# Optimization experiments

Measured on AMD Instinct MI355X. Metric: run time of the kernel, lower is better.

Reference implementation:

```python
import jax, jax.numpy as jnp
import numpy as np

DM = 1024        # model dim
E = 32           # totalexperts = expertsets*nexperts = 8*4
FE = 128         # expertsize
T = 4            # sparsity = nexperts (tokens per group)
EPS_TIEBREAK = 1e-6


def setup_inputs() -> dict:
    key = jax.random.key(0)
    k0, k1, k2, k3 = jax.random.split(key, 4)
    x = jax.random.normal(k0, (4, 4096, DM), dtype=jnp.float32)
    # fan_in-style inits matching misc.get_init_weight / get_init_bias
    controller = jax.random.normal(k1, (DM, E), dtype=jnp.float32) / np.float32(np.sqrt(DM))
    f1 = jax.random.normal(k2, (DM, E, FE), dtype=jnp.float32) / np.float32(np.sqrt(DM))
    bias = jnp.zeros((E, FE), dtype=jnp.float32)
    f2 = jax.random.normal(k3, (E, FE, DM), dtype=jnp.float32) / np.float32(np.sqrt(E * FE / T))
    return {"x": x, "controller": controller, "f1": f1, "bias": bias, "f2": f2}


def reference(x, controller, f1, bias, f2):
    B, S, d = x.shape
    t = T
    g = S // t
    # '... (b t) d -> ... b t d'
    grouped = x.reshape(B, g, t, d)
    # controller logits: '... t d, d e -> ... t e'
    logits = jnp.einsum('bgtd,de->bgte', grouped, controller)
    # deterministic tie-break offset over the t (slot) axis
    logits = logits + jnp.linspace(0.0, EPS_TIEBREAK, t, dtype=logits.dtype)[:, None]
    # softmax over dim=1 (group axis) as in original
    probs = jax.nn.softmax(logits, axis=1)
    # hard argmax mask over dim=-3 (group axis), scaled by soft probs
    perm = (logits == jnp.max(logits, axis=1, keepdims=True)).astype(x.dtype) * probs
    # expert up-projection with soft permutation: '... t d, d e f, ... t e -> ... e f'
    inner = jnp.einsum('bgtd,def,bgte->bgef', grouped, f1, perm)
    inner = jax.nn.relu(inner + bias)
    # expert down-projection: '... e f, e f d -> ... e d'
    inter = jnp.einsum('bgef,efd->bged', inner, f2)
    # unpermute: '... e d, ... t e -> ... t d'
    res = jnp.einsum('bged,bgte->bgtd', inter, perm)
    return res.reshape(B, S, d)
```

## Files before the change

### kernel.cpp

```cpp
#include <hip/hip_runtime.h>
#include <math.h>


#define DM   1024
#define NE   32
#define FE   128
#define T4   4
#define SS   4096
#define NGRP 1024
#define NROW 512
#define LP_STRIDE (NROW * NGRP)
#define VP_OFF   524288

__global__ __launch_bounds__(128, 2)
void k_logits(const float* __restrict__ x, const float* __restrict__ ctrl,
              float* __restrict__ Lp, float* __restrict__ out)
{
    const int m      = blockIdx.x;
    const int ks     = blockIdx.y;
    const int tid    = threadIdx.x;
    const int base_s = m * 128;
    const int b      = base_s >> 12;
    const int g0     = (base_s & 4095) >> 2;

    __shared__ float xT[64 * 132];
    __shared__ float cs[64 * 32];

    const int tq = tid & 31;
    const int eg = tid >> 5;

    float acc[4][8];
#pragma unroll
    for (int i = 0; i < 4; ++i)
#pragma unroll
        for (int j = 0; j < 8; ++j) acc[i][j] = 0.f;

    const int srow = tid >> 4;
    const int scol = tid & 15;

    for (int kit = 0; kit < 4; ++kit) {
        const int k0 = ks * 256 + kit * 64;
        __syncthreads();
#pragma unroll
        for (int p = 0; p < 16; ++p) {
            const int row = p * 8 + srow;
            const float4 v = *(const float4*)(x + (size_t)(base_s + row) * DM + k0 + scol * 4);
            const int d = scol * 4;
            xT[(d + 0) * 132 + row] = v.x;
            xT[(d + 1) * 132 + row] = v.y;
            xT[(d + 2) * 132 + row] = v.z;
            xT[(d + 3) * 132 + row] = v.w;
        }
        {
            const float4* cg = (const float4*)(ctrl + (size_t)k0 * NE);
            float4* cl = (float4*)cs;
            cl[tid]       = cg[tid];
            cl[tid + 128] = cg[tid + 128];
            cl[tid + 256] = cg[tid + 256];
            cl[tid + 384] = cg[tid + 384];
        }
        __syncthreads();

#pragma unroll 4
        for (int d = 0; d < 64; ++d) {
            const float4 xv = *(const float4*)(xT + d * 132 + tq * 4);
            const float4 c0 = *(const float4*)(cs + d * 32 + eg * 8);
            const float4 c1 = *(const float4*)(cs + d * 32 + eg * 8 + 4);
            const float xa[4] = { xv.x, xv.y, xv.z, xv.w };
            const float ca[8] = { c0.x, c0.y, c0.z, c0.w, c1.x, c1.y, c1.z, c1.w };
#pragma unroll
            for (int i = 0; i < 4; ++i)
#pragma unroll
                for (int j = 0; j < 8; ++j) acc[i][j] += xa[i] * ca[j];
        }
    }

    {
        float* Lb = Lp + (size_t)ks * LP_STRIDE;
        const int g = g0 + tq;
#pragma unroll
        for (int i = 0; i < 4; ++i)
#pragma unroll
            for (int j = 0; j < 8; ++j) {
                const int row = (b * T4 + i) * NE + eg * 8 + j;
                Lb[(size_t)row * NGRP + g] = acc[i][j];
            }
    }

    {
        const float4 z = make_float4(0.f, 0.f, 0.f, 0.f);
        float4* o4 = (float4*)(out + (size_t)(base_s + ks * 32) * DM);
#pragma unroll 8
        for (int i = tid; i < 32 * DM / 4; i += 128) o4[i] = z;
    }
}

__global__ __launch_bounds__(64)
void k_route(float* __restrict__ Lp)
{
    const int r    = blockIdx.x;
    const int lane = threadIdx.x;
    const float* L0 = Lp + (size_t)r * NGRP;

    float mx = -INFINITY, s = 0.f;
    int gm = 0;
#pragma unroll
    for (int c = 0; c < 4; ++c) {
        const int g0c = c * 256 + lane * 4;
        const float4 v0 = *(const float4*)(L0 + g0c);
        const float4 v1 = *(const float4*)(L0 + 1 * LP_STRIDE + g0c);
        const float4 v2 = *(const float4*)(L0 + 2 * LP_STRIDE + g0c);
        const float4 v3 = *(const float4*)(L0 + 3 * LP_STRIDE + g0c);
        const float l[4] = { v0.x + v1.x + v2.x + v3.x,
                             v0.y + v1.y + v2.y + v3.y,
                             v0.z + v1.z + v2.z + v3.z,
                             v0.w + v1.w + v2.w + v3.w };
#pragma unroll
        for (int j = 0; j < 4; ++j) {
            const float lv = l[j];
            if (lv > mx) { s = s * __expf(mx - lv) + 1.f; mx = lv; gm = g0c + j; }
            else         { s += __expf(lv - mx); }
        }
    }
#pragma unroll
    for (int off = 1; off < 64; off <<= 1) {
        const float m2 = __shfl_xor(mx, off);
        const float s2 = __shfl_xor(s, off);
        const int   g2 = __shfl_xor(gm, off);
        const float mn = fmaxf(mx, m2);
        s  = s * __expf(mx - mn) + s2 * __expf(m2 - mn);
        gm = (m2 > mx) ? g2 : ((m2 == mx && g2 < gm) ? g2 : gm);
        mx = mn;
    }
    if (lane == 0) {
        ((int*)Lp)[(size_t)r * NGRP] = gm;
        Lp[(size_t)r * NGRP + 1] = 1.f / s;
    }
}

__global__ __launch_bounds__(256, 2)
void k_up(const float* __restrict__ x, const float* __restrict__ f1,
          float* __restrict__ ws)
{
    const int e   = blockIdx.x & 31;
    const int dc  = blockIdx.x >> 5;
    const int tid = threadIdx.x;

    __shared__ float xs[16 * 68];
    __shared__ int   gS[16];

    if (tid < 16) {
        const int r = tid * NE + e;
        gS[tid] = ((const int*)ws)[(size_t)r * NGRP];
    }
    __syncthreads();

    {
        const int row = tid >> 4;
        const int f4c = tid & 15;
        const int bq = row >> 2, t = row & 3;
        const int s = bq * SS + gS[row] * 4 + t;
        const float4 v = *(const float4*)(x + (size_t)s * DM + dc * 64 + f4c * 4);
        xs[row * 68 + f4c * 4 + 0] = v.x;
        xs[row * 68 + f4c * 4 + 1] = v.y;
        xs[row * 68 + f4c * 4 + 2] = v.z;
        xs[row * 68 + f4c * 4 + 3] = v.w;
    }
    __syncthreads();

    const int f4 = tid & 31;
    const int rw = tid >> 5;
    const float* f1p = f1 + (size_t)(dc * 64) * (NE * FE) + e * FE + f4 * 4;
    const float* x0 = xs + rw * 68;
    const float* x1 = xs + (rw + 8) * 68;

    float a0[4] = {0.f, 0.f, 0.f, 0.f}, a1[4] = {0.f, 0.f, 0.f, 0.f};
#pragma unroll 16
    for (int dl = 0; dl < 64; ++dl) {
        const float4 w4 = *(const float4*)(f1p + (size_t)dl * (NE * FE));
        const float xa = x0[dl], xb = x1[dl];
        a0[0] += xa * w4.x; a0[1] += xa * w4.y; a0[2] += xa * w4.z; a0[3] += xa * w4.w;
        a1[0] += xb * w4.x; a1[1] += xb * w4.y; a1[2] += xb * w4.z; a1[3] += xb * w4.w;
    }

    float* Vp = ws + VP_OFF + (size_t)(dc * 32 + e) * (16 * FE);
    *(float4*)(Vp + rw       * FE + f4 * 4) = make_float4(a0[0], a0[1], a0[2], a0[3]);
    *(float4*)(Vp + (rw + 8) * FE + f4 * 4) = make_float4(a1[0], a1[1], a1[2], a1[3]);
}

__global__ __launch_bounds__(256, 2)
void k_down(const float* __restrict__ f2, const float* __restrict__ bias,
            const float* __restrict__ ws, float* __restrict__ out)
{
    const int e   = blockIdx.x & 31;
    const int dt  = (blockIdx.x >> 5) & 7;
    const int rh  = blockIdx.x >> 8;
    const int tid = threadIdx.x;

    __shared__ float vv[8 * 132];
    __shared__ float hs[8 * 132];
    __shared__ int   gS[8];
    __shared__ float pS[8];

    if (tid < 8) {
        const int r = (rh * 8 + tid) * NE + e;
        gS[tid] = ((const int*)ws)[(size_t)r * NGRP];
        pS[tid] = ws[(size_t)r * NGRP + 1];
    }

    {
        const float* Vp = ws + VP_OFF;
        const int row = tid >> 5, f4 = tid & 31;
        float4 s = make_float4(0.f, 0.f, 0.f, 0.f);
#pragma unroll
        for (int dc = 0; dc < 16; ++dc) {
            const float4 v = *(const float4*)(Vp + (size_t)(dc * 32 + e) * (16 * FE)
                                                 + (rh * 8 + row) * FE + f4 * 4);
            s.x += v.x; s.y += v.y; s.z += v.z; s.w += v.w;
        }
        *(float4*)(vv + row * 132 + f4 * 4) = s;
    }
    __syncthreads();

    {
#pragma unroll
        for (int q = 0; q < 4; ++q) {
            const int idx = tid + q * 256;
            const int row = idx >> 7, f = idx & 127;
            const int qb = row & ~3;
            float u = bias[e * FE + f];
#pragma unroll
            for (int t2 = 0; t2 < T4; ++t2)
                if (gS[qb + t2] == gS[row]) u += pS[qb + t2] * vv[(qb + t2) * 132 + f];
            hs[row * 132 + f] = pS[row] * fmaxf(u, 0.f);
        }
    }
    __syncthreads();

    const int d4 = tid & 31;
    const int rw = tid >> 5;
    const float* f2p = f2 + (size_t)e * FE * DM + dt * 128 + d4 * 4;
    const float* hp  = hs + rw * 132;

    float a[4] = {0.f, 0.f, 0.f, 0.f};
#pragma unroll 16
    for (int f = 0; f < FE; ++f) {
        const float4 w4 = *(const float4*)(f2p + (size_t)f * DM);
        const float ha = hp[f];
        a[0] += ha * w4.x; a[1] += ha * w4.y; a[2] += ha * w4.z; a[3] += ha * w4.w;
    }

    const int grow = rh * 8 + rw;
    const int bq = grow >> 2, t = grow & 3;
    float* orow = out + ((size_t)(bq * SS + gS[rw] * 4 + t)) * DM + dt * 128 + d4 * 4;
    atomicAdd(orow + 0, a[0]);
    atomicAdd(orow + 1, a[1]);
    atomicAdd(orow + 2, a[2]);
    atomicAdd(orow + 3, a[3]);
}

extern "C" void kernel_launch(void* const* d_in, const int* in_sizes, int n_in,
                              void* d_out, int out_size, void* d_ws, size_t ws_size,
                              hipStream_t stream)
{
    const float* x    = (const float*)d_in[0];
    const float* ctrl = (const float*)d_in[1];
    const float* f1   = (const float*)d_in[2];
    const float* bias = (const float*)d_in[3];
    const float* f2   = (const float*)d_in[4];
    float* out = (float*)d_out;
    float* ws  = (float*)d_ws;

    k_logits<<<dim3(128, 4), 128, 0, stream>>>(x, ctrl, ws, out);
    k_route <<<dim3(512),     64, 0, stream>>>(ws);
    k_up    <<<dim3(512),    256, 0, stream>>>(x, f1, ws);
    k_down  <<<dim3(512),    256, 0, stream>>>(f2, bias, ws, out);
}
```

Before: 202.3 us.

## Fuse four MoE stages into one cooperative kernel with grid syncs

Replaces the four separate launches (logits, route, up-projection, down-projection) with one cooperative kernel of 512 blocks x 256 threads that separates the stages with grid.sync(). The stage buffers share shared memory through a union. The logits stage is re-tiled for 256 threads with a 4x4 per-thread accumulator. The route stage now uses 4 waves per row with a cross-wave reduction in shared memory. The goal is to remove launch overhead and gaps between kernels, at the cost of grid-wide barrier latency and a cooperative launch that needs all 512 blocks resident at once.

```diff
diff --git a/kernel.cpp b/kernel.cpp
--- a/kernel.cpp
+++ b/kernel.cpp
@@ -1,5 +1,8 @@
 #include <hip/hip_runtime.h>
+#include <hip/hip_cooperative_groups.h>
 #include <math.h>
+
+namespace cg = cooperative_groups;
 
 
 #define DM   1024
@@ -12,101 +15,106 @@
 #define LP_STRIDE (NROW * NGRP)
 #define VP_OFF   524288
 
-__global__ __launch_bounds__(128, 2)
-void k_logits(const float* __restrict__ x, const float* __restrict__ ctrl,
-              float* __restrict__ Lp, float* __restrict__ out)
+struct SM1 { float xT[64 * 132]; float cs[64 * 32]; };
+struct SM2 { float rmx[4]; float rs[4]; int rgm[4]; };
+struct SM3 { float xs[16 * 68]; int gS[16]; };
+struct SM4 { float vv[8 * 132]; float hs[8 * 132]; int gS[8]; float pS[8]; };
+union SMU { SM1 p1; SM2 p2; SM3 p3; SM4 p4; };
+
+__global__ __launch_bounds__(256, 2)
+void k_fused(const float* __restrict__ x, const float* __restrict__ ctrl,
+             const float* __restrict__ f1, const float* __restrict__ bias,
+             const float* __restrict__ f2, float* __restrict__ ws,
+             float* __restrict__ out)
 {
-    const int m      = blockIdx.x;
-    const int ks     = blockIdx.y;
-    const int tid    = threadIdx.x;
-    const int base_s = m * 128;
-    const int b      = base_s >> 12;
-    const int g0     = (base_s & 4095) >> 2;
-
-    __shared__ float xT[64 * 132];
-    __shared__ float cs[64 * 32];
-
-    const int tq = tid & 31;
-    const int eg = tid >> 5;
-
-    float acc[4][8];
-#pragma unroll
-    for (int i = 0; i < 4; ++i)
-#pragma unroll
-        for (int j = 0; j < 8; ++j) acc[i][j] = 0.f;
-
-    const int srow = tid >> 4;
-    const int scol = tid & 15;
-
-    for (int kit = 0; kit < 4; ++kit) {
-        const int k0 = ks * 256 + kit * 64;
-        __syncthreads();
-#pragma unroll
-        for (int p = 0; p < 16; ++p) {
-            const int row = p * 8 + srow;
-            const float4 v = *(const float4*)(x + (size_t)(base_s + row) * DM + k0 + scol * 4);
-            const int d = scol * 4;
-            xT[(d + 0) * 132 + row] = v.x;
-            xT[(d + 1) * 132 + row] = v.y;
-            xT[(d + 2) * 132 + row] = v.z;
-            xT[(d + 3) * 132 + row] = v.w;
-        }
-        {
-            const float4* cg = (const float4*)(ctrl + (size_t)k0 * NE);
-            float4* cl = (float4*)cs;
-            cl[tid]       = cg[tid];
-            cl[tid + 128] = cg[tid + 128];
-            cl[tid + 256] = cg[tid + 256];
-            cl[tid + 384] = cg[tid + 384];
-        }
-        __syncthreads();
-
+    __shared__ SMU sm;
+    cg::grid_group grid = cg::this_grid();
+    const int bid = blockIdx.x;
+    const int tid = threadIdx.x;
+
+    {
+        const int m      = bid >> 2;
+        const int ks     = bid & 3;
+        const int base_s = m * 128;
+        const int b      = base_s >> 12;
+        const int g0     = (base_s & 4095) >> 2;
+
+        const int tq = tid & 31;
+        const int eg = tid >> 5;
+
+        float acc[4][4];
+#pragma unroll
+        for (int i = 0; i < 4; ++i)
+#pragma unroll
+            for (int j = 0; j < 4; ++j) acc[i][j] = 0.f;
+
+        const int row0 = tid >> 2;
+        const int f4i  = tid & 3;
+
+        for (int kit = 0; kit < 4; ++kit) {
+            const int k0 = ks * 256 + kit * 64;
+            __syncthreads();
+#pragma unroll
+            for (int rr = 0; rr < 2; ++rr) {
+                const int row = row0 + rr * 64;
+                const float* xp = x + (size_t)(base_s + row) * DM + k0;
+#pragma unroll
+                for (int cr = 0; cr < 4; ++cr) {
+                    const int col = f4i + cr * 4;
+                    const float4 v = *(const float4*)(xp + col * 4);
+                    const int d = col * 4;
+                    sm.p1.xT[(d + 0) * 132 + row] = v.x;
+                    sm.p1.xT[(d + 1) * 132 + row] = v.y;
+                    sm.p1.xT[(d + 2) * 132 + row] = v.z;
+                    sm.p1.xT[(d + 3) * 132 + row] = v.w;
+                }
+            }
+            {
+                const float4* cg4 = (const float4*)(ctrl + (size_t)k0 * NE);
+                float4* cl = (float4*)sm.p1.cs;
+                cl[tid]       = cg4[tid];
+                cl[tid + 256] = cg4[tid + 256];
+            }
+            __syncthreads();
+#pragma unroll 8
+            for (int d = 0; d < 64; ++d) {
+                const float4 xv = *(const float4*)(sm.p1.xT + d * 132 + tq * 4);
+                const float4 cv = *(const float4*)(sm.p1.cs + d * 32 + eg * 4);
+                const float xa[4] = { xv.x, xv.y, xv.z, xv.w };
+                const float ca[4] = { cv.x, cv.y, cv.z, cv.w };
+#pragma unroll
+                for (int i = 0; i < 4; ++i)
+#pragma unroll
+                    for (int j = 0; j < 4; ++j) acc[i][j] += xa[i] * ca[j];
+            }
+        }
+
+        {
+            float* Lb = ws + (size_t)ks * LP_STRIDE;
+            const int g = g0 + tq;
+#pragma unroll
+            for (int i = 0; i < 4; ++i)
+#pragma unroll
+                for (int j = 0; j < 4; ++j) {
+                    const int row = (b * T4 + i) * NE + eg * 4 + j;
+                    Lb[(size_t)row * NGRP + g] = acc[i][j];
+                }
+        }
+
+        {
+            const float4 z = make_float4(0.f, 0.f, 0.f, 0.f);
+            float4* o4 = (float4*)(out + (size_t)(base_s + ks * 32) * DM);
 #pragma unroll 4
-        for (int d = 0; d < 64; ++d) {
-            const float4 xv = *(const float4*)(xT + d * 132 + tq * 4);
-            const float4 c0 = *(const float4*)(cs + d * 32 + eg * 8);
-            const float4 c1 = *(const float4*)(cs + d * 32 + eg * 8 + 4);
-            const float xa[4] = { xv.x, xv.y, xv.z, xv.w };
-            const float ca[8] = { c0.x, c0.y, c0.z, c0.w, c1.x, c1.y, c1.z, c1.w };
-#pragma unroll
-            for (int i = 0; i < 4; ++i)
-#pragma unroll
-                for (int j = 0; j < 8; ++j) acc[i][j] += xa[i] * ca[j];
-        }
-    }
-
-    {
-        float* Lb = Lp + (size_t)ks * LP_STRIDE;
-        const int g = g0 + tq;
-#pragma unroll
-        for (int i = 0; i < 4; ++i)
-#pragma unroll
-            for (int j = 0; j < 8; ++j) {
-                const int row = (b * T4 + i) * NE + eg * 8 + j;
-                Lb[(size_t)row * NGRP + g] = acc[i][j];
-            }
-    }
-
-    {
-        const float4 z = make_float4(0.f, 0.f, 0.f, 0.f);
-        float4* o4 = (float4*)(out + (size_t)(base_s + ks * 32) * DM);
-#pragma unroll 8
-        for (int i = tid; i < 32 * DM / 4; i += 128) o4[i] = z;
-    }
-}
-
-__global__ __launch_bounds__(64)
-void k_route(float* __restrict__ Lp)
-{
-    const int r    = blockIdx.x;
-    const int lane = threadIdx.x;
-    const float* L0 = Lp + (size_t)r * NGRP;
-
-    float mx = -INFINITY, s = 0.f;
-    int gm = 0;
-#pragma unroll
-    for (int c = 0; c < 4; ++c) {
-        const int g0c = c * 256 + lane * 4;
+            for (int i = tid; i < 32 * DM / 4; i += 256) o4[i] = z;
+        }
+    }
+
+    grid.sync();
+
+    {
+        const int r = bid;
+        const float* L0 = ws + (size_t)r * NGRP;
+        const int g0c = tid * 4;
         const float4 v0 = *(const float4*)(L0 + g0c);
         const float4 v1 = *(const float4*)(L0 + 1 * LP_STRIDE + g0c);
         const float4 v2 = *(const float4*)(L0 + 2 * LP_STRIDE + g0c);
@@ -115,148 +123,154 @@
                              v0.y + v1.y + v2.y + v3.y,
                              v0.z + v1.z + v2.z + v3.z,
                              v0.w + v1.w + v2.w + v3.w };
+        float mx = -INFINITY, s = 0.f;
+        int gm = 0;
 #pragma unroll
         for (int j = 0; j < 4; ++j) {
             const float lv = l[j];
             if (lv > mx) { s = s * __expf(mx - lv) + 1.f; mx = lv; gm = g0c + j; }
             else         { s += __expf(lv - mx); }
         }
-    }
-#pragma unroll
-    for (int off = 1; off < 64; off <<= 1) {
-        const float m2 = __shfl_xor(mx, off);
-        const float s2 = __shfl_xor(s, off);
-        const int   g2 = __shfl_xor(gm, off);
-        const float mn = fmaxf(mx, m2);
-        s  = s * __expf(mx - mn) + s2 * __expf(m2 - mn);
-        gm = (m2 > mx) ? g2 : ((m2 == mx && g2 < gm) ? g2 : gm);
-        mx = mn;
-    }
-    if (lane == 0) {
-        ((int*)Lp)[(size_t)r * NGRP] = gm;
-        Lp[(size_t)r * NGRP + 1] = 1.f / s;
-    }
-}
-
-__global__ __launch_bounds__(256, 2)
-void k_up(const float* __restrict__ x, const float* __restrict__ f1,
-          float* __restrict__ ws)
-{
-    const int e   = blockIdx.x & 31;
-    const int dc  = blockIdx.x >> 5;
-    const int tid = threadIdx.x;
-
-    __shared__ float xs[16 * 68];
-    __shared__ int   gS[16];
-
-    if (tid < 16) {
-        const int r = tid * NE + e;
-        gS[tid] = ((const int*)ws)[(size_t)r * NGRP];
-    }
-    __syncthreads();
-
-    {
-        const int row = tid >> 4;
-        const int f4c = tid & 15;
-        const int bq = row >> 2, t = row & 3;
-        const int s = bq * SS + gS[row] * 4 + t;
-        const float4 v = *(const float4*)(x + (size_t)s * DM + dc * 64 + f4c * 4);
-        xs[row * 68 + f4c * 4 + 0] = v.x;
-        xs[row * 68 + f4c * 4 + 1] = v.y;
-        xs[row * 68 + f4c * 4 + 2] = v.z;
-        xs[row * 68 + f4c * 4 + 3] = v.w;
-    }
-    __syncthreads();
-
-    const int f4 = tid & 31;
-    const int rw = tid >> 5;
-    const float* f1p = f1 + (size_t)(dc * 64) * (NE * FE) + e * FE + f4 * 4;
-    const float* x0 = xs + rw * 68;
-    const float* x1 = xs + (rw + 8) * 68;
-
-    float a0[4] = {0.f, 0.f, 0.f, 0.f}, a1[4] = {0.f, 0.f, 0.f, 0.f};
+#pragma unroll
+        for (int off = 1; off < 64; off <<= 1) {
+            const float m2 = __shfl_xor(mx, off);
+            const float s2 = __shfl_xor(s, off);
+            const int   g2 = __shfl_xor(gm, off);
+            const float mn = fmaxf(mx, m2);
+            s  = s * __expf(mx - mn) + s2 * __expf(m2 - mn);
+            gm = (m2 > mx) ? g2 : ((m2 == mx && g2 < gm) ? g2 : gm);
+            mx = mn;
+        }
+        __syncthreads();
+        if ((tid & 63) == 0) {
+            const int w = tid >> 6;
+            sm.p2.rmx[w] = mx; sm.p2.rs[w] = s; sm.p2.rgm[w] = gm;
+        }
+        __syncthreads();
+        if (tid == 0) {
+            float M = sm.p2.rmx[0], S = sm.p2.rs[0];
+            int   G = sm.p2.rgm[0];
+#pragma unroll
+            for (int wv = 1; wv < 4; ++wv) {
+                const float m2 = sm.p2.rmx[wv], s2 = sm.p2.rs[wv];
+                const int   g2 = sm.p2.rgm[wv];
+                const float mn = fmaxf(M, m2);
+                S = S * __expf(M - mn) + s2 * __expf(m2 - mn);
+                G = (m2 > M) ? g2 : ((m2 == M && g2 < G) ? g2 : G);
+                M = mn;
+            }
+            ((int*)ws)[(size_t)r * NGRP] = G;
+            ws[(size_t)r * NGRP + 1] = 1.f / S;
+        }
+    }
+
+    grid.sync();
+
+    {
+        const int e  = bid & 31;
+        const int dc = bid >> 5;
+        if (tid < 16) {
+            const int rr = tid * NE + e;
+            sm.p3.gS[tid] = ((const int*)ws)[(size_t)rr * NGRP];
+        }
+        __syncthreads();
+        {
+            const int row = tid >> 4;
+            const int f4c = tid & 15;
+            const int bq = row >> 2, t = row & 3;
+            const int sIdx = bq * SS + sm.p3.gS[row] * 4 + t;
+            const float4 v = *(const float4*)(x + (size_t)sIdx * DM + dc * 64 + f4c * 4);
+            sm.p3.xs[row * 68 + f4c * 4 + 0] = v.x;
+            sm.p3.xs[row * 68 + f4c * 4 + 1] = v.y;
+            sm.p3.xs[row * 68 + f4c * 4 + 2] = v.z;
+            sm.p3.xs[row * 68 + f4c * 4 + 3] = v.w;
+        }
+        __syncthreads();
+
+        const int f4 = tid & 31;
+        const int rw = tid >> 5;
+        const float* f1p = f1 + (size_t)(dc * 64) * (NE * FE) + e * FE + f4 * 4;
+        const float* x0 = sm.p3.xs + rw * 68;
+        const float* x1 = sm.p3.xs + (rw + 8) * 68;
+
+        float a0[4] = {0.f, 0.f, 0.f, 0.f}, a1[4] = {0.f, 0.f, 0.f, 0.f};
 #pragma unroll 16
-    for (int dl = 0; dl < 64; ++dl) {
-        const float4 w4 = *(const float4*)(f1p + (size_t)dl * (NE * FE));
-        const float xa = x0[dl], xb = x1[dl];
-        a0[0] += xa * w4.x; a0[1] += xa * w4.y; a0[2] += xa * w4.z; a0[3] += xa * w4.w;
-        a1[0] += xb * w4.x; a1[1] += xb * w4.y; a1[2] += xb * w4.z; a1[3] += xb * w4.w;
-    }
-
-    float* Vp = ws + VP_OFF + (size_t)(dc * 32 + e) * (16 * FE);
-    *(float4*)(Vp + rw       * FE + f4 * 4) = make_float4(a0[0], a0[1], a0[2], a0[3]);
-    *(float4*)(Vp + (rw + 8) * FE + f4 * 4) = make_float4(a1[0], a1[1], a1[2], a1[3]);
-}
-
-__global__ __launch_bounds__(256, 2)
-void k_down(const float* __restrict__ f2, const float* __restrict__ bias,
-            const float* __restrict__ ws, float* __restrict__ out)
-{
-    const int e   = blockIdx.x & 31;
-    const int dt  = (blockIdx.x >> 5) & 7;
-    const int rh  = blockIdx.x >> 8;
-    const int tid = threadIdx.x;
-
-    __shared__ float vv[8 * 132];
-    __shared__ float hs[8 * 132];
-    __shared__ int   gS[8];
-    __shared__ float pS[8];
-
-    if (tid < 8) {
-        const int r = (rh * 8 + tid) * NE + e;
-        gS[tid] = ((const int*)ws)[(size_t)r * NGRP];
-        pS[tid] = ws[(size_t)r * NGRP + 1];
-    }
-
-    {
-        const float* Vp = ws + VP_OFF;
-        const int row = tid >> 5, f4 = tid & 31;
-        float4 s = make_float4(0.f, 0.f, 0.f, 0.f);
-#pragma unroll
-        for (int dc = 0; dc < 16; ++dc) {
-            const float4 v = *(const float4*)(Vp + (size_t)(dc * 32 + e) * (16 * FE)
-                                                 + (rh * 8 + row) * FE + f4 * 4);
-            s.x += v.x; s.y += v.y; s.z += v.z; s.w += v.w;
-        }
-        *(float4*)(vv + row * 132 + f4 * 4) = s;
-    }
-    __syncthreads();
-
-    {
-#pragma unroll
-        for (int q = 0; q < 4; ++q) {
-            const int idx = tid + q * 256;
-            const int row = idx >> 7, f = idx & 127;
-            const int qb = row & ~3;
-            float u = bias[e * FE + f];
-#pragma unroll
-            for (int t2 = 0; t2 < T4; ++t2)
-                if (gS[qb + t2] == gS[row]) u += pS[qb + t2] * vv[(qb + t2) * 132 + f];
-            hs[row * 132 + f] = pS[row] * fmaxf(u, 0.f);
-        }
-    }
-    __syncthreads();
-
-    const int d4 = tid & 31;
-    const int rw = tid >> 5;
-    const float* f2p = f2 + (size_t)e * FE * DM + dt * 128 + d4 * 4;
-    const float* hp  = hs + rw * 132;
-
-    float a[4] = {0.f, 0.f, 0.f, 0.f};
+        for (int dl = 0; dl < 64; ++dl) {
+            const float4 w4 = *(const float4*)(f1p + (size_t)dl * (NE * FE));
+            const float xa = x0[dl], xb = x1[dl];
+            a0[0] += xa * w4.x; a0[1] += xa * w4.y; a0[2] += xa * w4.z; a0[3] += xa * w4.w;
+            a1[0] += xb * w4.x; a1[1] += xb * w4.y; a1[2] += xb * w4.z; a1[3] += xb * w4.w;
+        }
+
+        float* Vp = ws + VP_OFF + (size_t)(dc * 32 + e) * (16 * FE);
+        *(float4*)(Vp + rw       * FE + f4 * 4) = make_float4(a0[0], a0[1], a0[2], a0[3]);
+        *(float4*)(Vp + (rw + 8) * FE + f4 * 4) = make_float4(a1[0], a1[1], a1[2], a1[3]);
+    }
+
+    grid.sync();
+
+    {
+        const int e  = bid & 31;
+        const int dt = (bid >> 5) & 7;
+        const int rh = bid >> 8;
+
+        if (tid < 8) {
+            const int rr = (rh * 8 + tid) * NE + e;
+            sm.p4.gS[tid] = ((const int*)ws)[(size_t)rr * NGRP];
+            sm.p4.pS[tid] = ws[(size_t)rr * NGRP + 1];
+        }
+
+        {
+            const float* Vp = ws + VP_OFF;
+            const int row = tid >> 5, f4 = tid & 31;
+            float4 s = make_float4(0.f, 0.f, 0.f, 0.f);
+#pragma unroll
+            for (int dc = 0; dc < 16; ++dc) {
+                const float4 v = *(const float4*)(Vp + (size_t)(dc * 32 + e) * (16 * FE)
+                                                     + (rh * 8 + row) * FE + f4 * 4);
+                s.x += v.x; s.y += v.y; s.z += v.z; s.w += v.w;
+            }
+            *(float4*)(sm.p4.vv + row * 132 + f4 * 4) = s;
+        }
+        __syncthreads();
+
+        {
+#pragma unroll
+            for (int q = 0; q < 4; ++q) {
+                const int idx = tid + q * 256;
+                const int row = idx >> 7, f = idx & 127;
+                const int qb = row & ~3;
+                float u = bias[e * FE + f];
+#pragma unroll
+                for (int t2 = 0; t2 < T4; ++t2)
+                    if (sm.p4.gS[qb + t2] == sm.p4.gS[row])
+                        u += sm.p4.pS[qb + t2] * sm.p4.vv[(qb + t2) * 132 + f];
+                sm.p4.hs[row * 132 + f] = sm.p4.pS[row] * fmaxf(u, 0.f);
+            }
+        }
+        __syncthreads();
+
+        const int d4 = tid & 31;
+        const int rw = tid >> 5;
+        const float* f2p = f2 + (size_t)e * FE * DM + dt * 128 + d4 * 4;
+        const float* hp  = sm.p4.hs + rw * 132;
+
+        float a[4] = {0.f, 0.f, 0.f, 0.f};
 #pragma unroll 16
-    for (int f = 0; f < FE; ++f) {
-        const float4 w4 = *(const float4*)(f2p + (size_t)f * DM);
-        const float ha = hp[f];
-        a[0] += ha * w4.x; a[1] += ha * w4.y; a[2] += ha * w4.z; a[3] += ha * w4.w;
-    }
-
-    const int grow = rh * 8 + rw;
-    const int bq = grow >> 2, t = grow & 3;
-    float* orow = out + ((size_t)(bq * SS + gS[rw] * 4 + t)) * DM + dt * 128 + d4 * 4;
-    atomicAdd(orow + 0, a[0]);
-    atomicAdd(orow + 1, a[1]);
-    atomicAdd(orow + 2, a[2]);
-    atomicAdd(orow + 3, a[3]);
+        for (int f = 0; f < FE; ++f) {
+            const float4 w4 = *(const float4*)(f2p + (size_t)f * DM);
+            const float ha = hp[f];
+            a[0] += ha * w4.x; a[1] += ha * w4.y; a[2] += ha * w4.z; a[3] += ha * w4.w;
+        }
+
+        const int grow = rh * 8 + rw;
+        const int bq = grow >> 2, t = grow & 3;
+        float* orow = out + ((size_t)(bq * SS + sm.p4.gS[rw] * 4 + t)) * DM + dt * 128 + d4 * 4;
+        atomicAdd(orow + 0, a[0]);
+        atomicAdd(orow + 1, a[1]);
+        atomicAdd(orow + 2, a[2]);
+        atomicAdd(orow + 3, a[3]);
+    }
 }
 
 extern "C" void kernel_launch(void* const* d_in, const int* in_sizes, int n_in,
@@ -271,8 +285,8 @@
     float* out = (float*)d_out;
     float* ws  = (float*)d_ws;
 
-    k_logits<<<dim3(128, 4), 128, 0, stream>>>(x, ctrl, ws, out);
-    k_route <<<dim3(512),     64, 0, stream>>>(ws);
-    k_up    <<<dim3(512),    256, 0, stream>>>(x, f1, ws);
-    k_down  <<<dim3(512),    256, 0, stream>>>(f2, bias, ws, out);
+    void* args[] = { (void*)&x, (void*)&ctrl, (void*)&f1, (void*)&bias,
+                     (void*)&f2, (void*)&ws, (void*)&out };
+    hipLaunchCooperativeKernel((const void*)k_fused, dim3(512), dim3(256),
+                               args, 0, stream);
 }
```

Result: slower. 397.1 us (+96.3%).

## Double-buffer logits GEMM tiles and widen route reduction to 256 threads

Applied to the files above, without the earlier changes.

The logits kernel moves to 256 threads per block with 4x4 per-thread tiles and 32-wide K steps. Shared-memory tiles are double-buffered so global loads for the next step are held in registers while the current step is computed, which removes one barrier per iteration. The route kernel now uses 256 threads, so each thread handles one float4 column set, and wave results are combined through shared memory, giving more memory parallelism per row. In exchange there is more shared memory per block, and the small route kernel pays an extra barrier.

```diff
diff --git a/kernel.cpp b/kernel.cpp
--- a/kernel.cpp
+++ b/kernel.cpp
@@ -12,7 +12,7 @@
 #define LP_STRIDE (NROW * NGRP)
 #define VP_OFF   524288
 
-__global__ __launch_bounds__(128, 2)
+__global__ __launch_bounds__(256, 3)
 void k_logits(const float* __restrict__ x, const float* __restrict__ ctrl,
               float* __restrict__ Lp, float* __restrict__ out)
 {
@@ -23,56 +23,80 @@
     const int b      = base_s >> 12;
     const int g0     = (base_s & 4095) >> 2;
 
-    __shared__ float xT[64 * 132];
-    __shared__ float cs[64 * 32];
+    __shared__ float xT[2][32 * 132];
+    __shared__ float cs[2][32 * 32];
 
     const int tq = tid & 31;
     const int eg = tid >> 5;
 
-    float acc[4][8];
+    float acc[4][4];
 #pragma unroll
     for (int i = 0; i < 4; ++i)
 #pragma unroll
-        for (int j = 0; j < 8; ++j) acc[i][j] = 0.f;
-
-    const int srow = tid >> 4;
-    const int scol = tid & 15;
-
-    for (int kit = 0; kit < 4; ++kit) {
-        const int k0 = ks * 256 + kit * 64;
+        for (int j = 0; j < 4; ++j) acc[i][j] = 0.f;
+
+    const int srow = tid >> 1;
+    const int sq   = tid & 1;
+
+    float4 px[4];
+    float4 pc;
+
+    const float* xrow = x + (size_t)(base_s + srow) * DM + sq * 16;
+
+    {
+        const int k0 = ks * 256;
+#pragma unroll
+        for (int cr = 0; cr < 4; ++cr) px[cr] = *(const float4*)(xrow + k0 + cr * 4);
+        pc = ((const float4*)(ctrl + (size_t)k0 * NE))[tid];
+#pragma unroll
+        for (int cr = 0; cr < 4; ++cr) {
+            const int d = (sq * 4 + cr) * 4;
+            const float4 v = px[cr];
+            xT[0][(d + 0) * 132 + srow] = v.x;
+            xT[0][(d + 1) * 132 + srow] = v.y;
+            xT[0][(d + 2) * 132 + srow] = v.z;
+            xT[0][(d + 3) * 132 + srow] = v.w;
+        }
+        ((float4*)cs[0])[tid] = pc;
+    }
+    __syncthreads();
+
+    for (int kit = 0; kit < 8; ++kit) {
+        if (kit < 7) {
+            const int k0 = ks * 256 + (kit + 1) * 32;
+#pragma unroll
+            for (int cr = 0; cr < 4; ++cr) px[cr] = *(const float4*)(xrow + k0 + cr * 4);
+            pc = ((const float4*)(ctrl + (size_t)k0 * NE))[tid];
+        }
+
+        const float* xb = xT[kit & 1];
+        const float* cb = cs[kit & 1];
+#pragma unroll 8
+        for (int d = 0; d < 32; ++d) {
+            const float4 xv = *(const float4*)(xb + d * 132 + tq * 4);
+            const float4 cv = *(const float4*)(cb + d * 32 + eg * 4);
+            const float xa[4] = { xv.x, xv.y, xv.z, xv.w };
+            const float ca[4] = { cv.x, cv.y, cv.z, cv.w };
+#pragma unroll
+            for (int i = 0; i < 4; ++i)
+#pragma unroll
+                for (int j = 0; j < 4; ++j) acc[i][j] += xa[i] * ca[j];
+        }
+
+        if (kit < 7) {
+            const int nb = (kit + 1) & 1;
+#pragma unroll
+            for (int cr = 0; cr < 4; ++cr) {
+                const int d = (sq * 4 + cr) * 4;
+                const float4 v = px[cr];
+                xT[nb][(d + 0) * 132 + srow] = v.x;
+                xT[nb][(d + 1) * 132 + srow] = v.y;
+                xT[nb][(d + 2) * 132 + srow] = v.z;
+                xT[nb][(d + 3) * 132 + srow] = v.w;
+            }
+            ((float4*)cs[nb])[tid] = pc;
+        }
         __syncthreads();
-#pragma unroll
-        for (int p = 0; p < 16; ++p) {
-            const int row = p * 8 + srow;
-            const float4 v = *(const float4*)(x + (size_t)(base_s + row) * DM + k0 + scol * 4);
-            const int d = scol * 4;
-            xT[(d + 0) * 132 + row] = v.x;
-            xT[(d + 1) * 132 + row] = v.y;
-            xT[(d + 2) * 132 + row] = v.z;
-            xT[(d + 3) * 132 + row] = v.w;
-        }
-        {
-            const float4* cg = (const float4*)(ctrl + (size_t)k0 * NE);
-            float4* cl = (float4*)cs;
-            cl[tid]       = cg[tid];
-            cl[tid + 128] = cg[tid + 128];
-            cl[tid + 256] = cg[tid + 256];
-            cl[tid + 384] = cg[tid + 384];
-        }
-        __syncthreads();
-
-#pragma unroll 4
-        for (int d = 0; d < 64; ++d) {
-            const float4 xv = *(const float4*)(xT + d * 132 + tq * 4);
-            const float4 c0 = *(const float4*)(cs + d * 32 + eg * 8);
-            const float4 c1 = *(const float4*)(cs + d * 32 + eg * 8 + 4);
-            const float xa[4] = { xv.x, xv.y, xv.z, xv.w };
-            const float ca[8] = { c0.x, c0.y, c0.z, c0.w, c1.x, c1.y, c1.z, c1.w };
-#pragma unroll
-            for (int i = 0; i < 4; ++i)
-#pragma unroll
-                for (int j = 0; j < 8; ++j) acc[i][j] += xa[i] * ca[j];
-        }
     }
 
     {
@@ -81,8 +105,8 @@
 #pragma unroll
         for (int i = 0; i < 4; ++i)
 #pragma unroll
-            for (int j = 0; j < 8; ++j) {
-                const int row = (b * T4 + i) * NE + eg * 8 + j;
+            for (int j = 0; j < 4; ++j) {
+                const int row = (b * T4 + i) * NE + eg * 4 + j;
                 Lb[(size_t)row * NGRP + g] = acc[i][j];
             }
     }
@@ -90,37 +114,37 @@
     {
         const float4 z = make_float4(0.f, 0.f, 0.f, 0.f);
         float4* o4 = (float4*)(out + (size_t)(base_s + ks * 32) * DM);
-#pragma unroll 8
-        for (int i = tid; i < 32 * DM / 4; i += 128) o4[i] = z;
-    }
-}
-
-__global__ __launch_bounds__(64)
+#pragma unroll 4
+        for (int i = tid; i < 32 * DM / 4; i += 256) o4[i] = z;
+    }
+}
+
+__global__ __launch_bounds__(256)
 void k_route(float* __restrict__ Lp)
 {
-    const int r    = blockIdx.x;
-    const int lane = threadIdx.x;
+    __shared__ float rmx[4], rs[4];
+    __shared__ int   rgm[4];
+
+    const int r   = blockIdx.x;
+    const int tid = threadIdx.x;
     const float* L0 = Lp + (size_t)r * NGRP;
 
+    const int g0c = tid * 4;
+    const float4 v0 = *(const float4*)(L0 + g0c);
+    const float4 v1 = *(const float4*)(L0 + 1 * LP_STRIDE + g0c);
+    const float4 v2 = *(const float4*)(L0 + 2 * LP_STRIDE + g0c);
+    const float4 v3 = *(const float4*)(L0 + 3 * LP_STRIDE + g0c);
+    const float l[4] = { v0.x + v1.x + v2.x + v3.x,
+                         v0.y + v1.y + v2.y + v3.y,
+                         v0.z + v1.z + v2.z + v3.z,
+                         v0.w + v1.w + v2.w + v3.w };
     float mx = -INFINITY, s = 0.f;
     int gm = 0;
 #pragma unroll
-    for (int c = 0; c < 4; ++c) {
-        const int g0c = c * 256 + lane * 4;
-        const float4 v0 = *(const float4*)(L0 + g0c);
-        const float4 v1 = *(const float4*)(L0 + 1 * LP_STRIDE + g0c);
-        const float4 v2 = *(const float4*)(L0 + 2 * LP_STRIDE + g0c);
-        const float4 v3 = *(const float4*)(L0 + 3 * LP_STRIDE + g0c);
-        const float l[4] = { v0.x + v1.x + v2.x + v3.x,
-                             v0.y + v1.y + v2.y + v3.y,
-                             v0.z + v1.z + v2.z + v3.z,
-                             v0.w + v1.w + v2.w + v3.w };
-#pragma unroll
-        for (int j = 0; j < 4; ++j) {
-            const float lv = l[j];
-            if (lv > mx) { s = s * __expf(mx - lv) + 1.f; mx = lv; gm = g0c + j; }
-            else         { s += __expf(lv - mx); }
-        }
+    for (int j = 0; j < 4; ++j) {
+        const float lv = l[j];
+        if (lv > mx) { s = s * __expf(mx - lv) + 1.f; mx = lv; gm = g0c + j; }
+        else         { s += __expf(lv - mx); }
     }
 #pragma unroll
     for (int off = 1; off < 64; off <<= 1) {
@@ -132,9 +156,25 @@
         gm = (m2 > mx) ? g2 : ((m2 == mx && g2 < gm) ? g2 : gm);
         mx = mn;
     }
-    if (lane == 0) {
-        ((int*)Lp)[(size_t)r * NGRP] = gm;
-        Lp[(size_t)r * NGRP + 1] = 1.f / s;
+    if ((tid & 63) == 0) {
+        const int w = tid >> 6;
+        rmx[w] = mx; rs[w] = s; rgm[w] = gm;
+    }
+    __syncthreads();
+    if (tid == 0) {
+        float M = rmx[0], S = rs[0];
+        int   G = rgm[0];
+#pragma unroll
+        for (int wv = 1; wv < 4; ++wv) {
+            const float m2 = rmx[wv], s2 = rs[wv];
+            const int   g2 = rgm[wv];
+            const float mn = fmaxf(M, m2);
+            S = S * __expf(M - mn) + s2 * __expf(m2 - mn);
+            G = (m2 > M) ? g2 : ((m2 == M && g2 < G) ? g2 : G);
+            M = mn;
+        }
+        ((int*)Lp)[(size_t)r * NGRP] = G;
+        Lp[(size_t)r * NGRP + 1] = 1.f / S;
     }
 }
 
@@ -271,8 +311,8 @@
     float* out = (float*)d_out;
     float* ws  = (float*)d_ws;
 
-    k_logits<<<dim3(128, 4), 128, 0, stream>>>(x, ctrl, ws, out);
-    k_route <<<dim3(512),     64, 0, stream>>>(ws);
+    k_logits<<<dim3(128, 4), 256, 0, stream>>>(x, ctrl, ws, out);
+    k_route <<<dim3(512),    256, 0, stream>>>(ws);
     k_up    <<<dim3(512),    256, 0, stream>>>(x, f1, ws);
     k_down  <<<dim3(512),    256, 0, stream>>>(f2, bias, ws, out);
 }
```

After: 189.9 us. 1.07x faster.

## Split output zeroing into its own kernel and widen logits and route parallelism

Applied to the files above, without the earlier changes.

Output zeroing moves out of the logits kernel into a dedicated k_zero kernel. The logits kernel now runs twice as many 64-thread blocks, each covering 64 rows with a new thread-to-data mapping, to expose more parallelism. The route kernel uses 256 threads per row with a cross-wave reduction through shared memory instead of one wave looping four times. The cost is an extra kernel launch, and the per-wave memory loop in route is traded for a block-wide synchronization.

```diff
diff --git a/kernel.cpp b/kernel.cpp
--- a/kernel.cpp
+++ b/kernel.cpp
@@ -12,22 +12,31 @@
 #define LP_STRIDE (NROW * NGRP)
 #define VP_OFF   524288
 
-__global__ __launch_bounds__(128, 2)
+__global__ __launch_bounds__(256)
+void k_zero(float* __restrict__ out)
+{
+    const float4 z = make_float4(0.f, 0.f, 0.f, 0.f);
+    float4* o4 = (float4*)out + (size_t)blockIdx.x * 2048;
+#pragma unroll
+    for (int j = 0; j < 8; ++j) o4[j * 256 + threadIdx.x] = z;
+}
+
+__global__ __launch_bounds__(64)
 void k_logits(const float* __restrict__ x, const float* __restrict__ ctrl,
-              float* __restrict__ Lp, float* __restrict__ out)
+              float* __restrict__ Lp)
 {
     const int m      = blockIdx.x;
     const int ks     = blockIdx.y;
     const int tid    = threadIdx.x;
-    const int base_s = m * 128;
+    const int base_s = m * 64;
     const int b      = base_s >> 12;
     const int g0     = (base_s & 4095) >> 2;
 
-    __shared__ float xT[64 * 132];
+    __shared__ float xT[64 * 68];
     __shared__ float cs[64 * 32];
 
-    const int tq = tid & 31;
-    const int eg = tid >> 5;
+    const int tq = tid >> 2;
+    const int eg = tid & 3;
 
     float acc[4][8];
 #pragma unroll
@@ -35,35 +44,38 @@
 #pragma unroll
         for (int j = 0; j < 8; ++j) acc[i][j] = 0.f;
 
-    const int srow = tid >> 4;
-    const int scol = tid & 15;
+    const int row0 = tid >> 2;
+    const int f4i  = tid & 3;
 
     for (int kit = 0; kit < 4; ++kit) {
         const int k0 = ks * 256 + kit * 64;
         __syncthreads();
 #pragma unroll
-        for (int p = 0; p < 16; ++p) {
-            const int row = p * 8 + srow;
-            const float4 v = *(const float4*)(x + (size_t)(base_s + row) * DM + k0 + scol * 4);
-            const int d = scol * 4;
-            xT[(d + 0) * 132 + row] = v.x;
-            xT[(d + 1) * 132 + row] = v.y;
-            xT[(d + 2) * 132 + row] = v.z;
-            xT[(d + 3) * 132 + row] = v.w;
+        for (int rr = 0; rr < 4; ++rr) {
+            const int row = row0 + rr * 16;
+            const float* xp = x + (size_t)(base_s + row) * DM + k0;
+#pragma unroll
+            for (int cr = 0; cr < 4; ++cr) {
+                const int col = f4i + cr * 4;
+                const float4 v = *(const float4*)(xp + col * 4);
+                const int d = col * 4;
+                xT[(d + 0) * 68 + row] = v.x;
+                xT[(d + 1) * 68 + row] = v.y;
+                xT[(d + 2) * 68 + row] = v.z;
+                xT[(d + 3) * 68 + row] = v.w;
+            }
         }
         {
             const float4* cg = (const float4*)(ctrl + (size_t)k0 * NE);
             float4* cl = (float4*)cs;
-            cl[tid]       = cg[tid];
-            cl[tid + 128] = cg[tid + 128];
-            cl[tid + 256] = cg[tid + 256];
-            cl[tid + 384] = cg[tid + 384];
+#pragma unroll
+            for (int q = 0; q < 8; ++q) cl[tid + q * 64] = cg[tid + q * 64];
         }
         __syncthreads();
 
 #pragma unroll 4
         for (int d = 0; d < 64; ++d) {
-            const float4 xv = *(const float4*)(xT + d * 132 + tq * 4);
+            const float4 xv = *(const float4*)(xT + d * 68 + tq * 4);
             const float4 c0 = *(const float4*)(cs + d * 32 + eg * 8);
             const float4 c1 = *(const float4*)(cs + d * 32 + eg * 8 + 4);
             const float xa[4] = { xv.x, xv.y, xv.z, xv.w };
@@ -86,41 +98,34 @@
                 Lb[(size_t)row * NGRP + g] = acc[i][j];
             }
     }
-
-    {
-        const float4 z = make_float4(0.f, 0.f, 0.f, 0.f);
-        float4* o4 = (float4*)(out + (size_t)(base_s + ks * 32) * DM);
-#pragma unroll 8
-        for (int i = tid; i < 32 * DM / 4; i += 128) o4[i] = z;
-    }
-}
-
-__global__ __launch_bounds__(64)
+}
+
+__global__ __launch_bounds__(256)
 void k_route(float* __restrict__ Lp)
 {
-    const int r    = blockIdx.x;
-    const int lane = threadIdx.x;
+    __shared__ float rmx[4], rs[4];
+    __shared__ int   rgm[4];
+
+    const int r   = blockIdx.x;
+    const int tid = threadIdx.x;
     const float* L0 = Lp + (size_t)r * NGRP;
 
+    const int g0c = tid * 4;
+    const float4 v0 = *(const float4*)(L0 + g0c);
+    const float4 v1 = *(const float4*)(L0 + 1 * LP_STRIDE + g0c);
+    const float4 v2 = *(const float4*)(L0 + 2 * LP_STRIDE + g0c);
+    const float4 v3 = *(const float4*)(L0 + 3 * LP_STRIDE + g0c);
+    const float l[4] = { v0.x + v1.x + v2.x + v3.x,
+                         v0.y + v1.y + v2.y + v3.y,
+                         v0.z + v1.z + v2.z + v3.z,
+                         v0.w + v1.w + v2.w + v3.w };
     float mx = -INFINITY, s = 0.f;
     int gm = 0;
 #pragma unroll
-    for (int c = 0; c < 4; ++c) {
-        const int g0c = c * 256 + lane * 4;
-        const float4 v0 = *(const float4*)(L0 + g0c);
-        const float4 v1 = *(const float4*)(L0 + 1 * LP_STRIDE + g0c);
-        const float4 v2 = *(const float4*)(L0 + 2 * LP_STRIDE + g0c);
-        const float4 v3 = *(const float4*)(L0 + 3 * LP_STRIDE + g0c);
-        const float l[4] = { v0.x + v1.x + v2.x + v3.x,
-                             v0.y + v1.y + v2.y + v3.y,
-                             v0.z + v1.z + v2.z + v3.z,
-                             v0.w + v1.w + v2.w + v3.w };
-#pragma unroll
-        for (int j = 0; j < 4; ++j) {
-            const float lv = l[j];
-            if (lv > mx) { s = s * __expf(mx - lv) + 1.f; mx = lv; gm = g0c + j; }
-            else         { s += __expf(lv - mx); }
-        }
+    for (int j = 0; j < 4; ++j) {
+        const float lv = l[j];
+        if (lv > mx) { s = s * __expf(mx - lv) + 1.f; mx = lv; gm = g0c + j; }
+        else         { s += __expf(lv - mx); }
     }
 #pragma unroll
     for (int off = 1; off < 64; off <<= 1) {
@@ -132,9 +137,25 @@
         gm = (m2 > mx) ? g2 : ((m2 == mx && g2 < gm) ? g2 : gm);
         mx = mn;
     }
-    if (lane == 0) {
-        ((int*)Lp)[(size_t)r * NGRP] = gm;
-        Lp[(size_t)r * NGRP + 1] = 1.f / s;
+    if ((tid & 63) == 0) {
+        const int w = tid >> 6;
+        rmx[w] = mx; rs[w] = s; rgm[w] = gm;
+    }
+    __syncthreads();
+    if (tid == 0) {
+        float M = rmx[0], S = rs[0];
+        int   G = rgm[0];
+#pragma unroll
+        for (int wv = 1; wv < 4; ++wv) {
+            const float m2 = rmx[wv], s2 = rs[wv];
+            const int   g2 = rgm[wv];
+            const float mn = fmaxf(M, m2);
+            S = S * __expf(M - mn) + s2 * __expf(m2 - mn);
+            G = (m2 > M) ? g2 : ((m2 == M && g2 < G) ? g2 : G);
+            M = mn;
+        }
+        ((int*)Lp)[(size_t)r * NGRP] = G;
+        Lp[(size_t)r * NGRP + 1] = 1.f / S;
     }
 }
 
@@ -271,8 +292,9 @@
     float* out = (float*)d_out;
     float* ws  = (float*)d_ws;
 
-    k_logits<<<dim3(128, 4), 128, 0, stream>>>(x, ctrl, ws, out);
-    k_route <<<dim3(512),     64, 0, stream>>>(ws);
+    k_zero  <<<dim3(2048),   256, 0, stream>>>(out);
+    k_logits<<<dim3(256, 4),  64, 0, stream>>>(x, ctrl, ws);
+    k_route <<<dim3(512),    256, 0, stream>>>(ws);
     k_up    <<<dim3(512),    256, 0, stream>>>(x, f1, ws);
     k_down  <<<dim3(512),    256, 0, stream>>>(f2, bias, ws, out);
 }
```

New measurement: 200.6 us. About the same (-0.9%).
